# Performance work log

Measured on AMD Instinct MI355X. Metric: run time of the kernel, lower is better.

Reference implementation:

```python
import jax, jax.numpy as jnp
import numpy as np

BITS = 4
PACK = 32 // BITS  # 8 nibbles per int32
GROUPSIZE = 128
IN_F, OUT_F = 4096, 11008
N_GROUPS = IN_F // GROUPSIZE


def setup_inputs() -> dict:
    key = jax.random.key(0)
    k1, k2, k3, k4, k5 = jax.random.split(key, 5)
    x = jax.random.normal(k1, (8192, IN_F), dtype=jnp.float32)
    # packed int4 weights: 8 values per int32 along the infeatures axis
    qweight = jax.random.randint(k2, (IN_F // PACK, OUT_F), jnp.iinfo(jnp.int32).min,
                                 jnp.iinfo(jnp.int32).max, dtype=jnp.int32)
    # packed int4 zero points: 8 values per int32 along the outfeatures axis
    qzeros = jax.random.randint(k3, (N_GROUPS, OUT_F // PACK), jnp.iinfo(jnp.int32).min,
                                jnp.iinfo(jnp.int32).max, dtype=jnp.int32)
    # small positive per-group scales, as produced by GPTQ quantization
    scales = (jax.random.uniform(k4, (N_GROUPS, OUT_F), dtype=jnp.float32) * 0.01 + 0.001)
    g_idx = (jnp.arange(IN_F, dtype=jnp.int32) // GROUPSIZE).astype(jnp.int32)
    bias = jax.random.normal(k5, (OUT_F,), dtype=jnp.float32)
    return {"x": x, "qweight": qweight, "qzeros": qzeros, "scales": scales,
            "g_idx": g_idx, "bias": bias}


def _unpack_int4_rows(packed):
    # packed: [in/8, out] int32 -> [in, out] int32 nibbles
    shifts = (BITS * jnp.arange(PACK, dtype=jnp.int32))  # [8]
    nib = (packed[:, None, :] >> shifts[None, :, None]) & 0xF  # [in/8, 8, out]
    return nib.reshape(packed.shape[0] * PACK, packed.shape[1])


def _unpack_int4_cols(packed):
    # packed: [G, out/8] int32 -> [G, out] int32 nibbles
    shifts = (BITS * jnp.arange(PACK, dtype=jnp.int32))  # [8]
    nib = (packed[:, :, None] >> shifts[None, None, :]) & 0xF  # [G, out/8, 8]
    return nib.reshape(packed.shape[0], packed.shape[1] * PACK)


def reference(x, qweight, qzeros, scales, g_idx, bias):
    q = _unpack_int4_rows(qweight)            # [in, out] int4 values in [0,15]
    z = _unpack_int4_cols(qzeros) + 1         # pack() stored zeros-1; GPTQ dequant adds it back
    # per-input-channel group lookup via g_idx
    s = scales[g_idx]                         # [in, out]
    zf = z[g_idx].astype(jnp.float32)         # [in, out]
    w = (q.astype(jnp.float32) - zf) * s      # dequantized weight [in, out]
    out = jnp.matmul(x, w) + bias             # [tokens, out]
    return out
```

## Files before the change

### kernel.cpp

```cpp
#include <hip/hip_runtime.h>
#include <stdint.h>

#define TOKENS 8192
#define IN_F   4096
#define OUT_F  11008
#define GROUPSIZE 128

#define BM 256
#define BN 256
#define BK 64
#define NT  (IN_F / BK)
#define NBM (TOKENS / BM)
#define NBN (OUT_F / BN)
#define NWG (NBM * NBN)

typedef __attribute__((ext_vector_type(8))) short          bf16x8;
typedef __attribute__((ext_vector_type(4))) float          f32x4;
typedef __attribute__((ext_vector_type(8))) unsigned short u16x8;

static __device__ __forceinline__ unsigned short f2bf(float f) {
    union { float f; unsigned int u; } v; v.f = f;
    unsigned int u = v.u;
    u += 0x7fffu + ((u >> 16) & 1u);
    return (unsigned short)(u >> 16);
}

__global__ void cvt_x_kernel(const float* __restrict__ x,
                             unsigned short* __restrict__ xb) {
    int i = (blockIdx.x * 256 + threadIdx.x) * 8;
    const float4* p = (const float4*)(x + i);
    float4 a = p[0];
    float4 b = p[1];
    u16x8 o;
    o[0] = f2bf(a.x); o[1] = f2bf(a.y); o[2] = f2bf(a.z); o[3] = f2bf(a.w);
    o[4] = f2bf(b.x); o[5] = f2bf(b.y); o[6] = f2bf(b.z); o[7] = f2bf(b.w);
    *(u16x8*)(xb + i) = o;
}

__global__ void dequant_kernel(const int* __restrict__ qweight,
                               const int* __restrict__ qzeros,
                               const float* __restrict__ scales,
                               unsigned short* __restrict__ Wt) {
    const int t  = threadIdx.x;
    const int n  = blockIdx.x * 32 + (t >> 3);
    const int kp = blockIdx.y * 8 + (t & 7);
    const int g  = blockIdx.y >> 1;
    const float s  = scales[g * OUT_F + n];
    const int   zq = ((qzeros[g * (OUT_F / 8) + (n >> 3)] >> (4 * (n & 7))) & 0xF) + 1;
    const float zs = (float)zq * s;
    const int qw = qweight[kp * OUT_F + n];
    u16x8 o;
#pragma unroll
    for (int j = 0; j < 8; ++j)
        o[j] = f2bf(fmaf((float)((qw >> (4 * j)) & 0xF), s, -zs));
    *(u16x8*)(Wt + (size_t)n * IN_F + kp * 8) = o;
}

#define GLD16(gp, lp)                                                        \
    __builtin_amdgcn_global_load_lds(                                        \
        (const __attribute__((address_space(1))) unsigned int*)(gp),         \
        (__attribute__((address_space(3))) unsigned int*)(lp), 16, 0, 0)

#define BARRIER() do {                                                       \
    asm volatile("" ::: "memory");                                           \
    __builtin_amdgcn_s_barrier();                                            \
    asm volatile("" ::: "memory");                                           \
} while (0)

__global__ __launch_bounds__(512, 2) void gemm_bias_kernel(
    const unsigned short* __restrict__ A,
    const unsigned short* __restrict__ Bt,
    const float* __restrict__ bias,
    float* __restrict__ C) {
    extern __shared__ char smem_c[];

    const int tid = threadIdx.x;
    const int l   = tid & 63;
    const int w   = tid >> 6;
    const int wr  = w >> 2;
    const int wc  = w & 3;

    const int bid = blockIdx.x;
    const int swz = (bid & 7) * (NWG / 8) + (bid >> 3);
    const int m0  = (swz / NBN) * BM;
    const int n0  = (swz % NBN) * BN;

    const int sperm = ((l & 7) ^ (l >> 3)) * 8;
    const unsigned short* aG = A  + (size_t)(m0 + w * 16 + (l >> 3)) * IN_F + sperm;
    const unsigned short* bG = Bt + (size_t)(n0 + w * 16 + (l >> 3)) * IN_F + sperm;
    char* sA = smem_c + w * 2048 + l * 16;
    char* sB = sA + 32768;

#define STAGE_A(b, h, tt) do {                                               \
    GLD16(aG + (size_t)((h) * 128    ) * IN_F + (tt) * 64,                   \
          sA + (b) * 65536 + (h) * 16384);                                   \
    GLD16(aG + (size_t)((h) * 128 + 8) * IN_F + (tt) * 64,                   \
          sA + (b) * 65536 + (h) * 16384 + 1024);                            \
} while (0)
#define STAGE_B(b, h, tt) do {                                               \
    GLD16(bG + (size_t)((h) * 128    ) * IN_F + (tt) * 64,                   \
          sB + (b) * 65536 + (h) * 16384);                                   \
    GLD16(bG + (size_t)((h) * 128 + 8) * IN_F + (tt) * 64,                   \
          sB + (b) * 65536 + (h) * 16384 + 1024);                            \
} while (0)

    const unsigned short* LAe = (const unsigned short*)smem_c;
    const unsigned short* LBe = (const unsigned short*)(smem_c + 32768);
    const int c0   = (((l >> 4) ^ (l & 7)) * 8);
    const int c1   = c0 ^ 32;
    const int arow = (wr * 128 + (l & 15)) * 64;
    const int brow = (wc * 64  + (l & 15)) * 64;

    f32x4  acc[8][4] = {};
    bf16x8 afr[8][2], bfr[4][2];

#define RDA(p, mi) do {                                                      \
    afr[mi][0] = *(const bf16x8*)&(p)[arow + (mi) * 1024 + c0];              \
    afr[mi][1] = *(const bf16x8*)&(p)[arow + (mi) * 1024 + c1];              \
} while (0)
#define RDB(p, nj) do {                                                      \
    bfr[nj][0] = *(const bf16x8*)&(p)[brow + (nj) * 1024 + c0];              \
    bfr[nj][1] = *(const bf16x8*)&(p)[brow + (nj) * 1024 + c1];              \
} while (0)
#define MM(mi, nj, ks)                                                       \
    acc[mi][nj] = __builtin_amdgcn_mfma_f32_16x16x32_bf16(                   \
        afr[mi][ks], bfr[nj][ks], acc[mi][nj], 0, 0, 0)
#define QUAD(ma, mb) do {                                                    \
    __builtin_amdgcn_s_setprio(1);                                           \
    MM(ma,0,0); MM(ma,1,0); MM(ma,2,0); MM(ma,3,0);                          \
    MM(mb,0,0); MM(mb,1,0); MM(mb,2,0); MM(mb,3,0);                          \
    MM(ma,0,1); MM(ma,1,1); MM(ma,2,1); MM(ma,3,1);                          \
    MM(mb,0,1); MM(mb,1,1); MM(mb,2,1); MM(mb,3,1);                          \
    __builtin_amdgcn_s_setprio(0);                                           \
} while (0)

    STAGE_A(0, 0, 0); STAGE_A(0, 1, 0);
    STAGE_B(0, 0, 0); STAGE_B(0, 1, 0);
    STAGE_A(1, 0, 1); STAGE_A(1, 1, 1);
    asm volatile("s_waitcnt vmcnt(4)" ::: "memory");
    __builtin_amdgcn_sched_barrier(0);
    BARRIER();

    for (int t = 0; t < NT; ++t) {
        const int bt = t & 1;
        const int bo = bt ^ 1;
        const unsigned short* pA = LAe + bt * 32768;
        const unsigned short* pB = LBe + bt * 32768;

        RDB(pB, 0); RDB(pB, 1); RDB(pB, 2); RDB(pB, 3);
        RDA(pA, 0); RDA(pA, 1); RDA(pA, 2); RDA(pA, 3);
        if (t + 1 < NT) STAGE_B(bo, 0, t + 1);
        BARRIER();
        QUAD(0, 1);
        BARRIER();

        RDA(pA, 4); RDA(pA, 5); RDA(pA, 6); RDA(pA, 7);
        if (t + 1 < NT) STAGE_B(bo, 1, t + 1);
        BARRIER();
        asm volatile("s_waitcnt lgkmcnt(0)" ::: "memory");
        __builtin_amdgcn_sched_barrier(0);
        QUAD(2, 3);
        BARRIER();

        if (t + 2 < NT) STAGE_A(bt, 0, t + 2);
        __builtin_amdgcn_sched_barrier(0);
        QUAD(4, 5);
        BARRIER();

        if (t + 2 < NT) STAGE_A(bt, 1, t + 2);
        __builtin_amdgcn_sched_barrier(0);
        QUAD(6, 7);
        if (t < NT - 2)
            asm volatile("s_waitcnt vmcnt(4)" ::: "memory");
        else
            asm volatile("s_waitcnt vmcnt(0)" ::: "memory");
        __builtin_amdgcn_sched_barrier(0);
        BARRIER();
    }

    const int col = l & 15;
    const int r0  = (l >> 4) * 4;
#pragma unroll
    for (int nj = 0; nj < 4; ++nj) {
        const int n = n0 + wc * 64 + nj * 16 + col;
        const float bv = bias[n];
#pragma unroll
        for (int mi = 0; mi < 8; ++mi) {
            const int m = m0 + wr * 128 + mi * 16 + r0;
#pragma unroll
            for (int r = 0; r < 4; ++r)
                C[(size_t)(m + r) * OUT_F + n] = acc[mi][nj][r] + bv;
        }
    }
}

__global__ __launch_bounds__(256) void fallback_kernel(
    const float* __restrict__ x, const int* __restrict__ qweight,
    const int* __restrict__ qzeros, const float* __restrict__ scales,
    const float* __restrict__ bias, float* __restrict__ C) {
    const int n = blockIdx.x * 16 + (threadIdx.x & 15);
    const int m = blockIdx.y * 16 + (threadIdx.x >> 4);
    float acc = 0.f;
    const float* xr = x + (size_t)m * IN_F;
    for (int g = 0; g < IN_F / GROUPSIZE; ++g) {
        const float s  = scales[g * OUT_F + n];
        const float zs = s * (float)(((qzeros[g * (OUT_F / 8) + (n >> 3)]
                                       >> (4 * (n & 7))) & 0xF) + 1);
        for (int kp = g * 16; kp < g * 16 + 16; ++kp) {
            const int qw = qweight[kp * OUT_F + n];
#pragma unroll
            for (int j = 0; j < 8; ++j) {
                const float w = fmaf((float)((qw >> (4 * j)) & 0xF), s, -zs);
                acc = fmaf(xr[kp * 8 + j], w, acc);
            }
        }
    }
    C[(size_t)m * OUT_F + n] = acc + bias[n];
}

extern "C" void kernel_launch(void* const* d_in, const int* in_sizes, int n_in,
                              void* d_out, int out_size, void* d_ws, size_t ws_size,
                              hipStream_t stream) {
    const float* x       = (const float*)d_in[0];
    const int*   qweight = (const int*)  d_in[1];
    const int*   qzeros  = (const int*)  d_in[2];
    const float* scales  = (const float*)d_in[3];
    const float* bias    = (const float*)d_in[5];
    float* out = (float*)d_out;

    const size_t xb_bytes = (size_t)TOKENS * IN_F * sizeof(unsigned short);
    const size_t wt_bytes = (size_t)OUT_F  * IN_F * sizeof(unsigned short);

    if (ws_size >= xb_bytes + wt_bytes) {
        static bool attr_done = false;
        if (!attr_done) {
            (void)hipFuncSetAttribute((const void*)gemm_bias_kernel,
                                      hipFuncAttributeMaxDynamicSharedMemorySize,
                                      131072);
            attr_done = true;
        }
        unsigned short* xb = (unsigned short*)d_ws;
        unsigned short* Wt = (unsigned short*)((char*)d_ws + xb_bytes);
        cvt_x_kernel<<<(TOKENS * IN_F) / (256 * 8), 256, 0, stream>>>(x, xb);
        dequant_kernel<<<dim3(OUT_F / 32, IN_F / 8 / 8), 256, 0, stream>>>(
            qweight, qzeros, scales, Wt);
        gemm_bias_kernel<<<NWG, 512, 131072, stream>>>(xb, Wt, bias, out);
    } else {
        fallback_kernel<<<dim3(OUT_F / 16, TOKENS / 16), 256, 0, stream>>>(
            x, qweight, qzeros, scales, bias, out);
    }
}
```

Before: 1.082 ms.

## Restructure GEMM main loop to stream A fragments in pairs and reorder staging

The GEMM inner loop now reads A fragments two rows at a time into a small reused register set instead of holding all eight, which lowers register pressure. It also swaps which operand is prefetched one versus two tiles ahead, and adds an explicit LDS wait before each MFMA block. The dequant kernel now handles two packed words per thread and writes 32-byte vectors, halving its grid. The extra per-phase LDS waits and barriers may expose more latency, and the reordered vmcnt accounting has to stay correct for the new staging order.

```diff
diff --git a/kernel.cpp b/kernel.cpp
--- a/kernel.cpp
+++ b/kernel.cpp
@@ -14,9 +14,10 @@
 #define NBN (OUT_F / BN)
 #define NWG (NBM * NBN)
 
-typedef __attribute__((ext_vector_type(8))) short          bf16x8;
-typedef __attribute__((ext_vector_type(4))) float          f32x4;
-typedef __attribute__((ext_vector_type(8))) unsigned short u16x8;
+typedef __attribute__((ext_vector_type(8)))  short          bf16x8;
+typedef __attribute__((ext_vector_type(4)))  float          f32x4;
+typedef __attribute__((ext_vector_type(8)))  unsigned short u16x8;
+typedef __attribute__((ext_vector_type(16))) unsigned short u16x16;
 
 static __device__ __forceinline__ unsigned short f2bf(float f) {
     union { float f; unsigned int u; } v; v.f = f;
@@ -41,19 +42,22 @@
                                const int* __restrict__ qzeros,
                                const float* __restrict__ scales,
                                unsigned short* __restrict__ Wt) {
-    const int t  = threadIdx.x;
-    const int n  = blockIdx.x * 32 + (t >> 3);
-    const int kp = blockIdx.y * 8 + (t & 7);
-    const int g  = blockIdx.y >> 1;
+    const int t   = threadIdx.x;
+    const int n   = blockIdx.x * 32 + (t >> 3);
+    const int kp0 = blockIdx.y * 16 + (t & 7) * 2;
+    const int g   = blockIdx.y;
     const float s  = scales[g * OUT_F + n];
     const int   zq = ((qzeros[g * (OUT_F / 8) + (n >> 3)] >> (4 * (n & 7))) & 0xF) + 1;
     const float zs = (float)zq * s;
-    const int qw = qweight[kp * OUT_F + n];
-    u16x8 o;
-#pragma unroll
-    for (int j = 0; j < 8; ++j)
-        o[j] = f2bf(fmaf((float)((qw >> (4 * j)) & 0xF), s, -zs));
-    *(u16x8*)(Wt + (size_t)n * IN_F + kp * 8) = o;
+    const int qw0 = qweight[(size_t)kp0 * OUT_F + n];
+    const int qw1 = qweight[(size_t)(kp0 + 1) * OUT_F + n];
+    u16x16 o;
+#pragma unroll
+    for (int j = 0; j < 8; ++j) {
+        o[j]     = f2bf(fmaf((float)((qw0 >> (4 * j)) & 0xF), s, -zs));
+        o[j + 8] = f2bf(fmaf((float)((qw1 >> (4 * j)) & 0xF), s, -zs));
+    }
+    *(u16x16*)(Wt + (size_t)n * IN_F + kp0 * 8) = o;
 }
 
 #define GLD16(gp, lp)                                                        \
@@ -65,6 +69,11 @@
     asm volatile("" ::: "memory");                                           \
     __builtin_amdgcn_s_barrier();                                            \
     asm volatile("" ::: "memory");                                           \
+} while (0)
+
+#define LGKM0() do {                                                         \
+    asm volatile("s_waitcnt lgkmcnt(0)" ::: "memory");                       \
+    __builtin_amdgcn_sched_barrier(0);                                       \
 } while (0)
 
 __global__ __launch_bounds__(512, 2) void gemm_bias_kernel(
@@ -112,31 +121,36 @@
     const int brow = (wc * 64  + (l & 15)) * 64;
 
     f32x4  acc[8][4] = {};
-    bf16x8 afr[8][2], bfr[4][2];
-
-#define RDA(p, mi) do {                                                      \
-    afr[mi][0] = *(const bf16x8*)&(p)[arow + (mi) * 1024 + c0];              \
-    afr[mi][1] = *(const bf16x8*)&(p)[arow + (mi) * 1024 + c1];              \
+    bf16x8 a0[2], a1[2], bfr[4][2];
+
+#define RDA_PAIR(p, mi) do {                                                 \
+    a0[0] = *(const bf16x8*)&(p)[arow + (mi) * 1024 + c0];                   \
+    a0[1] = *(const bf16x8*)&(p)[arow + (mi) * 1024 + c1];                   \
+    a1[0] = *(const bf16x8*)&(p)[arow + ((mi) + 1) * 1024 + c0];             \
+    a1[1] = *(const bf16x8*)&(p)[arow + ((mi) + 1) * 1024 + c1];             \
 } while (0)
 #define RDB(p, nj) do {                                                      \
     bfr[nj][0] = *(const bf16x8*)&(p)[brow + (nj) * 1024 + c0];              \
     bfr[nj][1] = *(const bf16x8*)&(p)[brow + (nj) * 1024 + c1];              \
 } while (0)
-#define MM(mi, nj, ks)                                                       \
+#define MM0(mi, nj, ks)                                                      \
     acc[mi][nj] = __builtin_amdgcn_mfma_f32_16x16x32_bf16(                   \
-        afr[mi][ks], bfr[nj][ks], acc[mi][nj], 0, 0, 0)
-#define QUAD(ma, mb) do {                                                    \
+        a0[ks], bfr[nj][ks], acc[mi][nj], 0, 0, 0)
+#define MM1(mi, nj, ks)                                                      \
+    acc[mi][nj] = __builtin_amdgcn_mfma_f32_16x16x32_bf16(                   \
+        a1[ks], bfr[nj][ks], acc[mi][nj], 0, 0, 0)
+#define QUADP(e) do {                                                        \
     __builtin_amdgcn_s_setprio(1);                                           \
-    MM(ma,0,0); MM(ma,1,0); MM(ma,2,0); MM(ma,3,0);                          \
-    MM(mb,0,0); MM(mb,1,0); MM(mb,2,0); MM(mb,3,0);                          \
-    MM(ma,0,1); MM(ma,1,1); MM(ma,2,1); MM(ma,3,1);                          \
-    MM(mb,0,1); MM(mb,1,1); MM(mb,2,1); MM(mb,3,1);                          \
+    MM0(e,0,0); MM0(e,1,0); MM0(e,2,0); MM0(e,3,0);                          \
+    MM1((e)+1,0,0); MM1((e)+1,1,0); MM1((e)+1,2,0); MM1((e)+1,3,0);          \
+    MM0(e,0,1); MM0(e,1,1); MM0(e,2,1); MM0(e,3,1);                          \
+    MM1((e)+1,0,1); MM1((e)+1,1,1); MM1((e)+1,2,1); MM1((e)+1,3,1);          \
     __builtin_amdgcn_s_setprio(0);                                           \
 } while (0)
 
     STAGE_A(0, 0, 0); STAGE_A(0, 1, 0);
     STAGE_B(0, 0, 0); STAGE_B(0, 1, 0);
-    STAGE_A(1, 0, 1); STAGE_A(1, 1, 1);
+    STAGE_B(1, 0, 1); STAGE_B(1, 1, 1);
     asm volatile("s_waitcnt vmcnt(4)" ::: "memory");
     __builtin_amdgcn_sched_barrier(0);
     BARRIER();
@@ -148,31 +162,35 @@
         const unsigned short* pB = LBe + bt * 32768;
 
         RDB(pB, 0); RDB(pB, 1); RDB(pB, 2); RDB(pB, 3);
-        RDA(pA, 0); RDA(pA, 1); RDA(pA, 2); RDA(pA, 3);
-        if (t + 1 < NT) STAGE_B(bo, 0, t + 1);
-        BARRIER();
-        QUAD(0, 1);
-        BARRIER();
-
-        RDA(pA, 4); RDA(pA, 5); RDA(pA, 6); RDA(pA, 7);
-        if (t + 1 < NT) STAGE_B(bo, 1, t + 1);
-        BARRIER();
-        asm volatile("s_waitcnt lgkmcnt(0)" ::: "memory");
-        __builtin_amdgcn_sched_barrier(0);
-        QUAD(2, 3);
-        BARRIER();
-
-        if (t + 2 < NT) STAGE_A(bt, 0, t + 2);
-        __builtin_amdgcn_sched_barrier(0);
-        QUAD(4, 5);
-        BARRIER();
-
-        if (t + 2 < NT) STAGE_A(bt, 1, t + 2);
-        __builtin_amdgcn_sched_barrier(0);
-        QUAD(6, 7);
+        RDA_PAIR(pA, 0);
+        if (t + 1 < NT) STAGE_A(bo, 0, t + 1);
+        BARRIER();
+        LGKM0();
+        QUADP(0);
+        BARRIER();
+
+        RDA_PAIR(pA, 2);
+        if (t + 1 < NT) STAGE_A(bo, 1, t + 1);
+        BARRIER();
+        LGKM0();
+        QUADP(2);
+        BARRIER();
+
+        RDA_PAIR(pA, 4);
+        if (t + 2 < NT) STAGE_B(bt, 0, t + 2);
+        BARRIER();
+        LGKM0();
+        QUADP(4);
+        BARRIER();
+
+        RDA_PAIR(pA, 6);
+        if (t + 2 < NT) STAGE_B(bt, 1, t + 2);
+        BARRIER();
+        LGKM0();
+        QUADP(6);
         if (t < NT - 2)
             asm volatile("s_waitcnt vmcnt(4)" ::: "memory");
-        else
+        else if (t == NT - 2)
             asm volatile("s_waitcnt vmcnt(0)" ::: "memory");
         __builtin_amdgcn_sched_barrier(0);
         BARRIER();
@@ -242,7 +260,7 @@
         unsigned short* xb = (unsigned short*)d_ws;
         unsigned short* Wt = (unsigned short*)((char*)d_ws + xb_bytes);
         cvt_x_kernel<<<(TOKENS * IN_F) / (256 * 8), 256, 0, stream>>>(x, xb);
-        dequant_kernel<<<dim3(OUT_F / 32, IN_F / 8 / 8), 256, 0, stream>>>(
+        dequant_kernel<<<dim3(OUT_F / 32, IN_F / 8 / 16), 256, 0, stream>>>(
             qweight, qzeros, scales, Wt);
         gemm_bias_kernel<<<NWG, 512, 131072, stream>>>(xb, Wt, bias, out);
     } else {
```

Measured after the change: 1.080 ms. No clear change (-0.1%).
